# Performance work log

Hardware: AMD Instinct MI355X
Metric: run time of the kernel (lower is better)

Reference implementation:

```python
import jax, jax.numpy as jnp
import numpy as np

B, N, M, D = 8, 4096, 256, 1024
H, HD, ROT = 16, 64, 32  # heads, head_dim, rotary dim (partial_rotary_factor=0.5)
GRID_H = GRID_W = 64     # sqrt(N)
BASE = 10000


def rope_tables_2d(h, w, rot_dim, base=BASE, dtype=jnp.float32):
    # 2D rope: half the rotary channels encode height, half encode width.
    n_freq = rot_dim // 4
    inv = 1.0 / (base ** (jnp.arange(n_freq, dtype=jnp.float32) / n_freq))
    fh = jnp.arange(h, dtype=jnp.float32)[:, None] * inv          # [h, nf]
    fw = jnp.arange(w, dtype=jnp.float32)[:, None] * inv          # [w, nf]
    fh_g = jnp.broadcast_to(fh[:, None, :], (h, w, n_freq))
    fw_g = jnp.broadcast_to(fw[None, :, :], (h, w, n_freq))
    freqs = jnp.concatenate([fh_g, fw_g], -1).reshape(h * w, rot_dim // 2)
    emb = jnp.concatenate([freqs, freqs], -1)                     # [h*w, rot_dim]
    return jnp.cos(emb).astype(dtype), jnp.sin(emb).astype(dtype)


def rotate_half(x):
    x1, x2 = jnp.split(x, 2, axis=-1)
    return jnp.concatenate([-x2, x1], axis=-1)


def layernorm(x, w, b, eps=1e-5):
    mu = x.mean(-1, keepdims=True)
    var = ((x - mu) ** 2).mean(-1, keepdims=True)
    return (x - mu) * jax.lax.rsqrt(var + eps) * w + b


def setup_inputs() -> dict:
    key = jax.random.key(0)
    ks = jax.random.split(key, 5)
    inner = H * HD
    return {
        "x": jax.random.normal(ks[0], (B, N, D), jnp.float32),
        "latents": jax.random.normal(ks[1], (B, M, D), jnp.float32),
        "ln_x_w": jnp.ones((D,), jnp.float32),
        "ln_x_b": jnp.zeros((D,), jnp.float32),
        "ln_l_w": jnp.ones((D,), jnp.float32),
        "ln_l_b": jnp.zeros((D,), jnp.float32),
        "Wq": jax.random.normal(ks[2], (D, inner), jnp.float32) * (D ** -0.5),
        "Wkv": jax.random.normal(ks[3], (D, 2 * inner), jnp.float32) * (D ** -0.5),
        "Wo": jax.random.normal(ks[4], (inner, D), jnp.float32) * (inner ** -0.5),
    }


def reference(x, latents, ln_x_w, ln_x_b, ln_l_w, ln_l_b, Wq, Wkv, Wo):
    scale = HD ** -0.5
    xn = layernorm(x, ln_x_w, ln_x_b)
    ln = layernorm(latents, ln_l_w, ln_l_b)

    q = ln @ Wq                                   # [B, M, H*HD]
    kv_x = xn @ Wkv                               # [B, N, 2*H*HD]
    kv_l = ln @ Wkv                               # [B, M, 2*H*HD]
    k_x, v_x = jnp.split(kv_x, 2, axis=-1)
    k_l, v_l = jnp.split(kv_l, 2, axis=-1)

    def to_bhnd(t, L):
        return t.reshape(t.shape[0], L, H, HD).transpose(0, 2, 1, 3)

    q = to_bhnd(q, M)                             # [B, H, M, HD]
    k_x = to_bhnd(k_x, N)                         # [B, H, N, HD]
    v_x = to_bhnd(v_x, N)
    k_l = to_bhnd(k_l, M)
    v_l = to_bhnd(v_l, M)

    # partial 2D RoPE on input keys only (first ROT channels)
    cos, sin = rope_tables_2d(GRID_H, GRID_W, ROT)  # [N, ROT]
    k_rope, k_pass = k_x[..., :ROT], k_x[..., ROT:]
    k_rope = k_rope * cos + rotate_half(k_rope) * sin
    k_x = jnp.concatenate([k_rope, k_pass], axis=-1)

    k = jnp.concatenate([k_x, k_l], axis=2)       # [B, H, N+M, HD]
    v = jnp.concatenate([v_x, v_l], axis=2)

    sim = jnp.einsum('bhid,bhjd->bhij', q * scale, k)   # [B, H, M, N+M]
    attn = jax.nn.softmax(sim, axis=-1)
    out = jnp.einsum('bhij,bhjd->bhid', attn, v)        # [B, H, M, HD]
    out = out.transpose(0, 2, 1, 3).reshape(out.shape[0], M, H * HD)
    return out @ Wo                                      # [B, M, D]
```

## Files before the change

### kernel.cpp

```cpp
#include <hip/hip_runtime.h>
#include <hip/hip_bf16.h>

#define Bb 8
#define Nn 4096
#define Mm 256
#define Dd 1024
#define Hh 16
#define HDd 64
#define Ss 4352
#define INNERd 1024
#define SPLIT 8

typedef __attribute__((ext_vector_type(4))) float f32x4;
typedef __attribute__((ext_vector_type(8))) short short8;
typedef __attribute__((ext_vector_type(4))) int int4v;

__device__ __forceinline__ float bf2f(short u) {
  union { unsigned int i; float f; } c;
  c.i = ((unsigned int)(unsigned short)u) << 16;
  return c.f;
}
__device__ __forceinline__ short f2bf(float f) {
  union { float f; unsigned int i; } c; c.f = f;
  unsigned int x = c.i;
  x += 0x7fff + ((x >> 16) & 1);
  return (short)(x >> 16);
}
__device__ __forceinline__ void gload16(const short* g, short* l) {
  __builtin_amdgcn_global_load_lds(
      (const __attribute__((address_space(1))) void*)g,
      (__attribute__((address_space(3))) void*)l, 16, 0, 0);
}

__global__ void ln_bf16_kernel(const float* __restrict__ src,
                               const float* __restrict__ w,
                               const float* __restrict__ bvec,
                               short* __restrict__ dst) {
  int row = blockIdx.x;
  const float4* x4 = (const float4*)(src + (size_t)row * Dd);
  int t = threadIdx.x;
  float4 v = x4[t];
  float s  = v.x + v.y + v.z + v.w;
  float ss = v.x*v.x + v.y*v.y + v.z*v.z + v.w*v.w;
#pragma unroll
  for (int o = 1; o < 64; o <<= 1) {
    s  += __shfl_xor(s,  o, 64);
    ss += __shfl_xor(ss, o, 64);
  }
  __shared__ float red[8];
  int wv = t >> 6;
  if ((t & 63) == 0) { red[wv] = s; red[4 + wv] = ss; }
  __syncthreads();
  float tot  = red[0] + red[1] + red[2] + red[3];
  float tot2 = red[4] + red[5] + red[6] + red[7];
  float mean = tot * (1.0f / Dd);
  float var  = tot2 * (1.0f / Dd) - mean * mean;
  float inv  = rsqrtf(var + 1e-5f);
  float4 wv4 = ((const float4*)w)[t];
  float4 bv4 = ((const float4*)bvec)[t];
  short4 o4;
  o4.x = f2bf((v.x - mean) * inv * wv4.x + bv4.x);
  o4.y = f2bf((v.y - mean) * inv * wv4.y + bv4.y);
  o4.z = f2bf((v.z - mean) * inv * wv4.z + bv4.z);
  o4.w = f2bf((v.w - mean) * inv * wv4.w + bv4.w);
  *(short4*)(dst + (size_t)row * Dd + t * 4) = o4;
}

__global__ void wconv_kernel(const float* __restrict__ src, short* __restrict__ dst,
                             int K, int Ncol) {
  __shared__ float tile[32][33];
  int bx = blockIdx.x, by = blockIdx.y;
  int tx = threadIdx.x, ty = threadIdx.y;
#pragma unroll
  for (int i = 0; i < 32; i += 8)
    tile[ty + i][tx] = src[(size_t)(by * 32 + ty + i) * Ncol + bx * 32 + tx];
  __syncthreads();
#pragma unroll
  for (int i = 0; i < 32; i += 8)
    dst[(size_t)(bx * 32 + ty + i) * K + by * 32 + tx] = f2bf(tile[tx][ty + i]);
}

template<int MODE>
__global__ __launch_bounds__(256, 4) void gemm_bt_kernel(
    const short* __restrict__ A, const short* __restrict__ Bt,
    void* __restrict__ C0, short* __restrict__ kdst, short* __restrict__ vdst,
    int ncp) {
  __shared__ __align__(16) short Asm[128 * 64];
  __shared__ __align__(16) short Bsm[128 * 64];
  __shared__ float ctab[(MODE == 2) ? 1024 : 1];
  int t = threadIdx.x;
  int wave = t >> 6, lane = t & 63;
  int wm = (wave >> 1) * 64, wn = (wave & 1) * 64;
  int lr = lane & 15, lg = lane >> 4;
  int nwg = gridDim.x;
  int cpx = nwg >> 3;
  int swz = (blockIdx.x & 7) * cpx + (blockIdx.x >> 3);
  int colp = swz % ncp, rowp = swz / ncp;
  int brow = rowp * 128, bcol = colp * 128;
  if (MODE == 2) {
#pragma unroll
    for (int i = t; i < 512; i += 256) {
      int pos = i >> 3, f = i & 7;
      float ang = (float)pos * exp2f(-1.6609640474436813f * (float)f);
      ctab[i] = cosf(ang);
      ctab[512 + i] = sinf(ang);
    }
  }
  f32x4 acc[4][4] = {};
  for (int kt = 0; kt < 1024; kt += 64) {
    __syncthreads();
#pragma unroll
    for (int u = 0; u < 4; u++) {
      int cid = t + u * 256;
      int r = cid >> 3, c = cid & 7;
      int cl = c ^ (r & 7);
      gload16(A + (size_t)(brow + r) * 1024 + kt + cl * 8, Asm + cid * 8);
      gload16(Bt + (size_t)(bcol + r) * 1024 + kt + cl * 8, Bsm + cid * 8);
    }
    __syncthreads();
#pragma unroll
    for (int ks = 0; ks < 2; ks++) {
      short8 a[4], b[4];
#pragma unroll
      for (int i = 0; i < 4; i++) {
        int ra = wm + i * 16 + lr;
        a[i] = *(const short8*)(Asm + ra * 64 + (((ks * 4 + lg) ^ (ra & 7)) * 8));
        int rb = wn + i * 16 + lr;
        b[i] = *(const short8*)(Bsm + rb * 64 + (((ks * 4 + lg) ^ (rb & 7)) * 8));
      }
#pragma unroll
      for (int mi = 0; mi < 4; mi++)
#pragma unroll
        for (int ni = 0; ni < 4; ni++)
          acc[mi][ni] = __builtin_amdgcn_mfma_f32_16x16x32_bf16(a[mi], b[ni], acc[mi][ni], 0, 0, 0);
    }
  }
  int cbase = bcol + wn;
  bool kreg = (cbase & 2047) < 1024;
#pragma unroll
  for (int mi = 0; mi < 4; mi++)
#pragma unroll
    for (int rr = 0; rr < 4; rr++) {
      int row = brow + wm + mi * 16 + lg * 4 + rr;
      float v[4];
#pragma unroll
      for (int ni = 0; ni < 4; ni++) v[ni] = acc[mi][ni][rr];
      if (MODE == 0) {
        float* C = (float*)C0;
#pragma unroll
        for (int ni = 0; ni < 4; ni++)
          C[(size_t)row * 1024 + cbase + ni * 16 + lr] = v[ni];
      } else if (MODE == 2) {
        int bb = row >> 12, n = row & 4095;
        if (kreg) {
          int pos = (lr & 8) ? (n & 63) : (n >> 6);
          float cs = ctab[pos * 8 + (lr & 7)];
          float sn = ctab[512 + pos * 8 + (lr & 7)];
          float v0 = v[0], v1 = v[1];
          v[0] = v0 * cs - v1 * sn;
          v[1] = v1 * cs + v0 * sn;
        }
        short* dstp = kreg ? kdst : vdst;
        int h = (cbase & 1023) >> 6;
        size_t rb = (((size_t)(bb * Hh + h)) * Ss + n) * HDd;
#pragma unroll
        for (int ni = 0; ni < 4; ni++)
          dstp[rb + ni * 16 + lr] = f2bf(v[ni]);
      } else {
        int bb = row >> 8, m = row & 255;
        if (cbase < 1024) {
          int h = cbase >> 6;
          size_t rb = (((size_t)(bb * Hh + h)) * Mm + m) * HDd;
#pragma unroll
          for (int ni = 0; ni < 4; ni++)
            ((short*)C0)[rb + ni * 16 + lr] = f2bf(v[ni] * 0.125f);
        } else if (cbase < 2048) {
          int h = (cbase - 1024) >> 6;
          size_t rb = (((size_t)(bb * Hh + h)) * Ss + (Nn + m)) * HDd;
#pragma unroll
          for (int ni = 0; ni < 4; ni++)
            kdst[rb + ni * 16 + lr] = f2bf(v[ni]);
        } else {
          int h = (cbase - 2048) >> 6;
          size_t rb = (((size_t)(bb * Hh + h)) * Ss + (Nn + m)) * HDd;
#pragma unroll
          for (int ni = 0; ni < 4; ni++)
            vdst[rb + ni * 16 + lr] = f2bf(v[ni]);
        }
      }
    }
}

__global__ __launch_bounds__(512) void attn_kernel(const short* __restrict__ qb,
                            const short* __restrict__ kb,
                            const short* __restrict__ vb,
                            float* __restrict__ pO,
                            float* __restrict__ pS) {
  __shared__ __align__(16) short Ksm[64 * 64];
  __shared__ __align__(16) short Vsm[64 * 64];
  __shared__ __align__(16) short Psm[8][32 * 64];
  int blk = blockIdx.x;
  int sp = blk & (SPLIT - 1), bh = blk >> 3;
  int t = threadIdx.x, wave = t >> 6, lane = t & 63;
  int lr = lane & 15, lg = lane >> 4;
  int q0 = wave * 32;
  const short* qptr = qb + (size_t)bh * Mm * HDd;
  short8 qf[2][2];
#pragma unroll
  for (int mi = 0; mi < 2; mi++)
#pragma unroll
    for (int ks = 0; ks < 2; ks++)
      qf[mi][ks] = *(const short8*)(qptr + (size_t)(q0 + mi * 16 + lr) * HDd + ks * 32 + lg * 8);
  f32x4 accO[2][4] = {};
  float psum[2][4] = {};
  const short* kbase = kb + (size_t)bh * Ss * HDd;
  const short* vbase = vb + (size_t)bh * Ss * HDd;
  short* P = &Psm[wave][0];
  int tile0 = (sp * 68) >> 3, tile1 = ((sp + 1) * 68) >> 3;
  for (int tt = tile0; tt < tile1; tt++) {
    int kt = tt * 64;
    __syncthreads();
    {
      int r = t >> 3, c = t & 7;
      int cl = c ^ (r & 7);
      gload16(kbase + (size_t)(kt + r) * HDd + cl * 8, Ksm + t * 8);
      short8 vv = *(const short8*)(vbase + (size_t)(kt + r) * HDd + c * 8);
#pragma unroll
      for (int e = 0; e < 8; e++) {
        int d = c * 8 + e;
        Vsm[d * 64 + (((r >> 3) ^ (d & 7)) * 8) + (r & 7)] = vv[e];
      }
    }
    __syncthreads();
    f32x4 accS[2][4] = {};
#pragma unroll
    for (int ks = 0; ks < 2; ks++) {
      short8 bk[4];
#pragma unroll
      for (int ji = 0; ji < 4; ji++) {
        int j = ji * 16 + lr;
        int cd = ks * 4 + lg;
        bk[ji] = *(const short8*)(Ksm + j * 64 + ((cd ^ (j & 7)) * 8));
      }
#pragma unroll
      for (int mi = 0; mi < 2; mi++)
#pragma unroll
        for (int ji = 0; ji < 4; ji++)
          accS[mi][ji] = __builtin_amdgcn_mfma_f32_16x16x32_bf16(qf[mi][ks], bk[ji], accS[mi][ji], 0, 0, 0);
    }
#pragma unroll
    for (int mi = 0; mi < 2; mi++)
#pragma unroll
      for (int r = 0; r < 4; r++) {
        float rs = 0.0f;
#pragma unroll
        for (int ji = 0; ji < 4; ji++) {
          float pv = __expf(accS[mi][ji][r]);
          accS[mi][ji][r] = pv;
          rs += pv;
        }
        psum[mi][r] += rs;
      }
#pragma unroll
    for (int mi = 0; mi < 2; mi++)
#pragma unroll
      for (int ji = 0; ji < 4; ji++)
#pragma unroll
        for (int r = 0; r < 4; r++) {
          int row = mi * 16 + lg * 4 + r;
          int col = ji * 16 + lr;
          P[row * 64 + (((col >> 3) ^ (row & 7)) * 8) + (col & 7)] = f2bf(accS[mi][ji][r]);
        }
#pragma unroll
    for (int ks = 0; ks < 2; ks++) {
      short8 pa[2], bvv[4];
#pragma unroll
      for (int mi = 0; mi < 2; mi++) {
        int row = mi * 16 + lr;
        int ck = ks * 4 + lg;
        pa[mi] = *(const short8*)(P + row * 64 + ((ck ^ (row & 7)) * 8));
      }
#pragma unroll
      for (int di = 0; di < 4; di++) {
        int d = di * 16 + lr;
        int ck = ks * 4 + lg;
        bvv[di] = *(const short8*)(Vsm + d * 64 + ((ck ^ (d & 7)) * 8));
      }
#pragma unroll
      for (int mi = 0; mi < 2; mi++)
#pragma unroll
        for (int di = 0; di < 4; di++)
          accO[mi][di] = __builtin_amdgcn_mfma_f32_16x16x32_bf16(pa[mi], bvv[di], accO[mi][di], 0, 0, 0);
    }
  }
#pragma unroll
  for (int mi = 0; mi < 2; mi++)
#pragma unroll
    for (int r = 0; r < 4; r++) {
#pragma unroll
      for (int o = 1; o < 16; o <<= 1)
        psum[mi][r] += __shfl_xor(psum[mi][r], o, 64);
    }
  size_t base = (size_t)blk * 256;
#pragma unroll
  for (int mi = 0; mi < 2; mi++)
#pragma unroll
    for (int r = 0; r < 4; r++) {
      int m = q0 + mi * 16 + lg * 4 + r;
      if (lr == 0) pS[base + m] = psum[mi][r];
#pragma unroll
      for (int di = 0; di < 4; di++)
        pO[(base + m) * 64 + di * 16 + lr] = accO[mi][di][r];
    }
}

__global__ void attn_combine(const float* __restrict__ pO, const float* __restrict__ pS,
                             short* __restrict__ ob) {
  int t = threadIdx.x;
  int row = blockIdx.x * 4 + (t >> 6);
  int bh = row >> 8, m = row & 255;
  int d = t & 63;
  float den = 0.0f, acc = 0.0f;
#pragma unroll
  for (int s = 0; s < SPLIT; s++) {
    size_t rbase = ((size_t)(bh * SPLIT + s) * 256 + m);
    den += pS[rbase];
    acc += pO[rbase * 64 + d];
  }
  int b = bh >> 4, h = bh & 15;
  ob[((size_t)(b * Mm + m)) * INNERd + h * HDd + d] = f2bf(acc / den);
}

extern "C" void kernel_launch(void* const* d_in, const int* in_sizes, int n_in,
                              void* d_out, int out_size, void* d_ws, size_t ws_size,
                              hipStream_t stream) {
  const float* x    = (const float*)d_in[0];
  const float* lat  = (const float*)d_in[1];
  const float* lnxw = (const float*)d_in[2];
  const float* lnxb = (const float*)d_in[3];
  const float* lnlw = (const float*)d_in[4];
  const float* lnlb = (const float*)d_in[5];
  const float* Wq   = (const float*)d_in[6];
  const float* Wkv  = (const float*)d_in[7];
  const float* Wo   = (const float*)d_in[8];
  char* w = (char*)d_ws;
  const size_t MB = 1048576;
  short* Wqkvt = (short*)(w + 0 * MB);
  short* Wot   = (short*)(w + 6 * MB);
  short* xn    = (short*)(w + 8 * MB);
  short* lnr   = (short*)(w + 72 * MB);
  short* qbuf  = (short*)(w + 76 * MB);
  short* kbuf  = (short*)(w + 80 * MB);
  short* vbuf  = (short*)(w + 148 * MB);
  short* aout  = (short*)(w + 216 * MB);
  float* pO    = (float*)(w + 8 * MB);
  float* pS    = (float*)(w + 72 * MB);

  ln_bf16_kernel<<<dim3(Bb * Nn), dim3(256), 0, stream>>>(x, lnxw, lnxb, xn);
  ln_bf16_kernel<<<dim3(Bb * Mm), dim3(256), 0, stream>>>(lat, lnlw, lnlb, lnr);
  wconv_kernel<<<dim3(32, 32), dim3(32, 8), 0, stream>>>(Wq, Wqkvt, 1024, 1024);
  wconv_kernel<<<dim3(64, 32), dim3(32, 8), 0, stream>>>(Wkv, Wqkvt + (size_t)1024 * 1024, 1024, 2048);
  wconv_kernel<<<dim3(32, 32), dim3(32, 8), 0, stream>>>(Wo, Wot, 1024, 1024);
  gemm_bt_kernel<2><<<dim3(4096), dim3(256), 0, stream>>>(
      xn, Wqkvt + (size_t)1024 * 1024, nullptr, kbuf, vbuf, 16);
  gemm_bt_kernel<4><<<dim3(384), dim3(256), 0, stream>>>(
      lnr, Wqkvt, (void*)qbuf, kbuf, vbuf, 24);
  attn_kernel<<<dim3(Bb * Hh * SPLIT), dim3(512), 0, stream>>>(qbuf, kbuf, vbuf, pO, pS);
  attn_combine<<<dim3(Bb * Hh * Mm / 4), dim3(256), 0, stream>>>(pO, pS, aout);
  gemm_bt_kernel<0><<<dim3(128), dim3(256), 0, stream>>>(
      aout, Wot, d_out, nullptr, nullptr, 8);
}
```

Measured before the change: 340.5 us.

## Compute transposed S and O in attention to keep P in registers

The attention kernel now computes S^T = K·Q^T, so the MFMA output layout of the softmax probabilities matches the B-operand layout for the P·V product. This removes the per-wave shared-memory P buffer and its write/read round trip. The V shared-memory swizzle is changed to match the new k-ordering of the packed P fragments. Partial outputs are stored transposed (d-major) and the combine kernel is rewritten so each thread handles one query row with 32 dims and does vectorized bf16 stores, at the cost of more registers per thread and fewer, larger combine blocks.

```diff
diff --git a/kernel.cpp b/kernel.cpp
--- a/kernel.cpp
+++ b/kernel.cpp
@@ -198,7 +198,6 @@
                             float* __restrict__ pS) {
   __shared__ __align__(16) short Ksm[64 * 64];
   __shared__ __align__(16) short Vsm[64 * 64];
-  __shared__ __align__(16) short Psm[8][32 * 64];
   int blk = blockIdx.x;
   int sp = blk & (SPLIT - 1), bh = blk >> 3;
   int t = threadIdx.x, wave = t >> 6, lane = t & 63;
@@ -207,15 +206,14 @@
   const short* qptr = qb + (size_t)bh * Mm * HDd;
   short8 qf[2][2];
 #pragma unroll
-  for (int mi = 0; mi < 2; mi++)
+  for (int qi = 0; qi < 2; qi++)
 #pragma unroll
     for (int ks = 0; ks < 2; ks++)
-      qf[mi][ks] = *(const short8*)(qptr + (size_t)(q0 + mi * 16 + lr) * HDd + ks * 32 + lg * 8);
-  f32x4 accO[2][4] = {};
-  float psum[2][4] = {};
+      qf[qi][ks] = *(const short8*)(qptr + (size_t)(q0 + qi * 16 + lr) * HDd + ks * 32 + lg * 8);
+  f32x4 accOT[4][2] = {};
+  float psq[2] = {0.0f, 0.0f};
   const short* kbase = kb + (size_t)bh * Ss * HDd;
   const short* vbase = vb + (size_t)bh * Ss * HDd;
-  short* P = &Psm[wave][0];
   int tile0 = (sp * 68) >> 3, tile1 = ((sp + 1) * 68) >> 3;
   for (int tt = tile0; tt < tile1; tt++) {
     int kt = tt * 64;
@@ -225,110 +223,112 @@
       int cl = c ^ (r & 7);
       gload16(kbase + (size_t)(kt + r) * HDd + cl * 8, Ksm + t * 8);
       short8 vv = *(const short8*)(vbase + (size_t)(kt + r) * HDd + c * 8);
+      int sc = ((r >> 5) << 2) | ((r >> 2) & 3);
+      int sw = (((r >> 4) & 1) << 2) | (r & 3);
 #pragma unroll
       for (int e = 0; e < 8; e++) {
         int d = c * 8 + e;
-        Vsm[d * 64 + (((r >> 3) ^ (d & 7)) * 8) + (r & 7)] = vv[e];
+        Vsm[d * 64 + ((sc ^ (d & 7)) * 8) + sw] = vv[e];
       }
     }
     __syncthreads();
-    f32x4 accS[2][4] = {};
+    f32x4 accST[4][2] = {};
 #pragma unroll
     for (int ks = 0; ks < 2; ks++) {
-      short8 bk[4];
+      short8 ka[4];
 #pragma unroll
       for (int ji = 0; ji < 4; ji++) {
         int j = ji * 16 + lr;
         int cd = ks * 4 + lg;
-        bk[ji] = *(const short8*)(Ksm + j * 64 + ((cd ^ (j & 7)) * 8));
-      }
-#pragma unroll
-      for (int mi = 0; mi < 2; mi++)
-#pragma unroll
-        for (int ji = 0; ji < 4; ji++)
-          accS[mi][ji] = __builtin_amdgcn_mfma_f32_16x16x32_bf16(qf[mi][ks], bk[ji], accS[mi][ji], 0, 0, 0);
-    }
-#pragma unroll
-    for (int mi = 0; mi < 2; mi++)
-#pragma unroll
-      for (int r = 0; r < 4; r++) {
-        float rs = 0.0f;
-#pragma unroll
-        for (int ji = 0; ji < 4; ji++) {
-          float pv = __expf(accS[mi][ji][r]);
-          accS[mi][ji][r] = pv;
-          rs += pv;
+        ka[ji] = *(const short8*)(Ksm + j * 64 + ((cd ^ (j & 7)) * 8));
+      }
+#pragma unroll
+      for (int ji = 0; ji < 4; ji++)
+#pragma unroll
+        for (int qi = 0; qi < 2; qi++)
+          accST[ji][qi] = __builtin_amdgcn_mfma_f32_16x16x32_bf16(ka[ji], qf[qi][ks], accST[ji][qi], 0, 0, 0);
+    }
+    short8 pb[2][2];
+#pragma unroll
+    for (int qi = 0; qi < 2; qi++) {
+#pragma unroll
+      for (int ji = 0; ji < 4; ji++)
+#pragma unroll
+        for (int r = 0; r < 4; r++) {
+          float pv = __expf(accST[ji][qi][r]);
+          accST[ji][qi][r] = pv;
+          psq[qi] += pv;
         }
-        psum[mi][r] += rs;
-      }
-#pragma unroll
-    for (int mi = 0; mi < 2; mi++)
-#pragma unroll
-      for (int ji = 0; ji < 4; ji++)
+#pragma unroll
+      for (int s = 0; s < 2; s++)
 #pragma unroll
         for (int r = 0; r < 4; r++) {
-          int row = mi * 16 + lg * 4 + r;
-          int col = ji * 16 + lr;
-          P[row * 64 + (((col >> 3) ^ (row & 7)) * 8) + (col & 7)] = f2bf(accS[mi][ji][r]);
+          pb[s][qi][r]     = f2bf(accST[2 * s][qi][r]);
+          pb[s][qi][4 + r] = f2bf(accST[2 * s + 1][qi][r]);
         }
-#pragma unroll
-    for (int ks = 0; ks < 2; ks++) {
-      short8 pa[2], bvv[4];
-#pragma unroll
-      for (int mi = 0; mi < 2; mi++) {
-        int row = mi * 16 + lr;
-        int ck = ks * 4 + lg;
-        pa[mi] = *(const short8*)(P + row * 64 + ((ck ^ (row & 7)) * 8));
-      }
+    }
+#pragma unroll
+    for (int s = 0; s < 2; s++) {
+      short8 va[4];
 #pragma unroll
       for (int di = 0; di < 4; di++) {
         int d = di * 16 + lr;
-        int ck = ks * 4 + lg;
-        bvv[di] = *(const short8*)(Vsm + d * 64 + ((ck ^ (d & 7)) * 8));
-      }
-#pragma unroll
-      for (int mi = 0; mi < 2; mi++)
-#pragma unroll
-        for (int di = 0; di < 4; di++)
-          accO[mi][di] = __builtin_amdgcn_mfma_f32_16x16x32_bf16(pa[mi], bvv[di], accO[mi][di], 0, 0, 0);
-    }
-  }
-#pragma unroll
-  for (int mi = 0; mi < 2; mi++)
-#pragma unroll
-    for (int r = 0; r < 4; r++) {
-#pragma unroll
-      for (int o = 1; o < 16; o <<= 1)
-        psum[mi][r] += __shfl_xor(psum[mi][r], o, 64);
-    }
+        int ck = s * 4 + lg;
+        va[di] = *(const short8*)(Vsm + d * 64 + ((ck ^ (d & 7)) * 8));
+      }
+#pragma unroll
+      for (int di = 0; di < 4; di++)
+#pragma unroll
+        for (int qi = 0; qi < 2; qi++)
+          accOT[di][qi] = __builtin_amdgcn_mfma_f32_16x16x32_bf16(va[di], pb[s][qi], accOT[di][qi], 0, 0, 0);
+    }
+  }
+#pragma unroll
+  for (int qi = 0; qi < 2; qi++) {
+    psq[qi] += __shfl_xor(psq[qi], 16, 64);
+    psq[qi] += __shfl_xor(psq[qi], 32, 64);
+  }
   size_t base = (size_t)blk * 256;
-#pragma unroll
-  for (int mi = 0; mi < 2; mi++)
-#pragma unroll
-    for (int r = 0; r < 4; r++) {
-      int m = q0 + mi * 16 + lg * 4 + r;
-      if (lr == 0) pS[base + m] = psum[mi][r];
-#pragma unroll
-      for (int di = 0; di < 4; di++)
-        pO[(base + m) * 64 + di * 16 + lr] = accO[mi][di][r];
-    }
+  if (lane < 16) {
+#pragma unroll
+    for (int qi = 0; qi < 2; qi++)
+      pS[base + q0 + qi * 16 + lr] = psq[qi];
+  }
+  float* poB = pO + base * 64;
+#pragma unroll
+  for (int di = 0; di < 4; di++)
+#pragma unroll
+    for (int qi = 0; qi < 2; qi++)
+#pragma unroll
+      for (int r = 0; r < 4; r++)
+        poB[(size_t)(di * 16 + lg * 4 + r) * 256 + q0 + qi * 16 + lr] = accOT[di][qi][r];
 }
 
 __global__ void attn_combine(const float* __restrict__ pO, const float* __restrict__ pS,
                              short* __restrict__ ob) {
-  int t = threadIdx.x;
-  int row = blockIdx.x * 4 + (t >> 6);
-  int bh = row >> 8, m = row & 255;
-  int d = t & 63;
-  float den = 0.0f, acc = 0.0f;
+  int blk = blockIdx.x;
+  int bh = blk >> 1, dh = (blk & 1) << 5;
+  int q = threadIdx.x;
+  float den = 0.0f;
+  float acc[32] = {};
 #pragma unroll
   for (int s = 0; s < SPLIT; s++) {
-    size_t rbase = ((size_t)(bh * SPLIT + s) * 256 + m);
-    den += pS[rbase];
-    acc += pO[rbase * 64 + d];
-  }
+    size_t b2 = (size_t)(bh * SPLIT + s);
+    den += pS[b2 * 256 + q];
+    const float* po = pO + b2 * 16384 + (size_t)dh * 256;
+#pragma unroll
+    for (int d = 0; d < 32; d++) acc[d] += po[d * 256 + q];
+  }
+  float rden = 1.0f / den;
   int b = bh >> 4, h = bh & 15;
-  ob[((size_t)(b * Mm + m)) * INNERd + h * HDd + d] = f2bf(acc / den);
+  short* dst = ob + ((size_t)(b * Mm + q)) * INNERd + h * HDd + dh;
+#pragma unroll
+  for (int c = 0; c < 4; c++) {
+    short8 o8;
+#pragma unroll
+    for (int e = 0; e < 8; e++) o8[e] = f2bf(acc[c * 8 + e] * rden);
+    *(short8*)(dst + c * 8) = o8;
+  }
 }
 
 extern "C" void kernel_launch(void* const* d_in, const int* in_sizes, int n_in,
@@ -366,7 +366,7 @@
   gemm_bt_kernel<4><<<dim3(384), dim3(256), 0, stream>>>(
       lnr, Wqkvt, (void*)qbuf, kbuf, vbuf, 24);
   attn_kernel<<<dim3(Bb * Hh * SPLIT), dim3(512), 0, stream>>>(qbuf, kbuf, vbuf, pO, pS);
-  attn_combine<<<dim3(Bb * Hh * Mm / 4), dim3(256), 0, stream>>>(pO, pS, aout);
+  attn_combine<<<dim3(256), dim3(256), 0, stream>>>(pO, pS, aout);
   gemm_bt_kernel<0><<<dim3(128), dim3(256), 0, stream>>>(
       aout, Wot, d_out, nullptr, nullptr, 8);
 }
```

New measurement: 314.0 us. 7.8% less time.
